# Optimization experiments

Hardware: AMD Instinct MI355X
Metric: run time of the kernel (lower is better)

## Reference

```python
import jax, jax.numpy as jnp
import numpy as np

D_MODEL = 512
NUM_HEADS = 8
HEAD_DIM = D_MODEL // NUM_HEADS


def setup_inputs() -> dict:
    key = jax.random.key(0)
    ks = jax.random.split(key, 11)
    N, S, D = 2, 4096, D_MODEL
    s = 1.0 / np.sqrt(D)
    return {
        "query": jax.random.normal(ks[0], (N, S, D), jnp.float32),
        "key": jax.random.normal(ks[1], (N, S, D), jnp.float32),
        "value": jax.random.normal(ks[2], (N, S, D), jnp.float32),
        "Wq": jax.random.normal(ks[3], (D, D), jnp.float32) * s,
        "bq": jnp.zeros((D,), jnp.float32),
        "Wk": jax.random.normal(ks[4], (D, D), jnp.float32) * s,
        "bk": jnp.zeros((D,), jnp.float32),
        "Wv": jax.random.normal(ks[5], (D, D), jnp.float32) * s,
        "bv": jnp.zeros((D,), jnp.float32),
        "Wo": jax.random.normal(ks[6], (D, D), jnp.float32) * s,
        "bo": jnp.zeros((D,), jnp.float32),
    }


def reference(query, key, value, Wq, bq, Wk, bk, Wv, bv, Wo, bo):
    N, S, D = query.shape
    H, Hd = NUM_HEADS, HEAD_DIM
    # Linear projections (torch Linear: x @ W.T + b), split heads -> [N,H,S,Hd]
    Q = (query @ Wq.T + bq).reshape(N, S, H, Hd).transpose(0, 2, 1, 3)
    K = (key @ Wk.T + bk).reshape(N, S, H, Hd).transpose(0, 2, 1, 3)
    V = (value @ Wv.T + bv).reshape(N, S, H, Hd).transpose(0, 2, 1, 3)
    scale = 1.0 / np.sqrt(Hd)
    energy = jnp.einsum("nhqd,nhkd->nhqk", Q, K) * scale  # [N,H,S,S]
    attention = jax.nn.softmax(energy, axis=-1)
    out = jnp.einsum("nhqk,nhkd->nhqd", attention, V)
    out = out.transpose(0, 2, 1, 3).reshape(N, S, D)
    return out @ Wo.T + bo
```

## Files before the change

kernel.cpp:

```cpp
#include <hip/hip_runtime.h>


#define SEQ 4096
#define PERHEAD 262144
#define CEXPF 0.18033688011112042f

typedef short bf16x8 __attribute__((ext_vector_type(8)));
typedef short bf16x4 __attribute__((ext_vector_type(4)));
typedef float f32x4 __attribute__((ext_vector_type(4)));
typedef unsigned short u16;
typedef unsigned int u32;

__device__ inline float bf2f(u16 h) {
    return __uint_as_float(((u32)h) << 16);
}
__device__ inline u16 f2bf(float f) {
    u32 u = __float_as_uint(f);
    u = (u + 0x7fffu + ((u >> 16) & 1u)) >> 16;
    return (u16)u;
}
__device__ inline u32 packtrunc(float lo, float hi) {
    return __builtin_amdgcn_perm(__float_as_uint(hi), __float_as_uint(lo),
                                 0x07060302u);
}
__device__ inline uint4 pack8(float4 a, float4 b) {
    uint4 r;
    r.x = (u32)f2bf(a.x) | ((u32)f2bf(a.y) << 16);
    r.y = (u32)f2bf(a.z) | ((u32)f2bf(a.w) << 16);
    r.z = (u32)f2bf(b.x) | ((u32)f2bf(b.y) << 16);
    r.w = (u32)f2bf(b.z) | ((u32)f2bf(b.w) << 16);
    return r;
}

__global__ void detect_dtype(const u16* __restrict__ W, int* __restrict__ flag) {
    const int lane = threadIdx.x & 63;
    u16 u = W[2 * lane];
    int e = (u >> 7) & 0xFF;
    int plaus = (u == 0) || (e >= 100 && e <= 132);
    unsigned long long m = __ballot(plaus);
    if (lane == 0) *flag = (__popcll(m) >= 48) ? 0 : 1;
}

__global__ __launch_bounds__(256) void prep(
    const void* __restrict__ W0, const void* __restrict__ W1,
    const void* __restrict__ W2, const void* __restrict__ W3,
    const void* __restrict__ b0, const void* __restrict__ b1,
    const void* __restrict__ b2, const void* __restrict__ b3,
    u16* __restrict__ Wc, u16* __restrict__ bc, const int* __restrict__ flag)
{
    const int m = blockIdx.y;
    const void* Ws = (m == 0) ? W0 : (m == 1) ? W1 : (m == 2) ? W2 : W3;
    const void* bs = (m == 0) ? b0 : (m == 1) ? b1 : (m == 2) ? b2 : b3;
    const int isf32 = *flag;
    if (blockIdx.x < 128) {
        const int idx = blockIdx.x * 2048 + threadIdx.x * 8;
        u16* dst = Wc + (size_t)m * 262144 + idx;
        if (isf32) {
            const float4* s = (const float4*)((const float*)Ws + idx);
            *(uint4*)dst = pack8(s[0], s[1]);
        } else {
            *(uint4*)dst = *(const uint4*)((const u16*)Ws + idx);
        }
    } else if (threadIdx.x < 64) {
        const int idx = threadIdx.x * 8;
        u16* dst = bc + m * 512 + idx;
        if (isf32) {
            const float4* s = (const float4*)((const float*)bs + idx);
            *(uint4*)dst = pack8(s[0], s[1]);
        } else {
            *(uint4*)dst = *(const uint4*)((const u16*)bs + idx);
        }
    }
}

template <int A_BF16>
__device__ inline void gemm_body(
    const void* __restrict__ Av, const u16* __restrict__ B,
    const u16* __restrict__ bias, void* __restrict__ outv,
    int isf32, int mode, float scale, int m0, int n0,
    u16* As, u16* Bs)
{
    const int tid = threadIdx.x;
    const int wave = tid >> 6, lane = tid & 63, quad = lane >> 4, ln = lane & 15;
    const int qr = wave >> 1, qc = wave & 1;

    f32x4 acc[4][4];
#pragma unroll
    for (int i = 0; i < 4; i++)
#pragma unroll
        for (int j = 0; j < 4; j++) acc[i][j] = (f32x4){0.f, 0.f, 0.f, 0.f};

    const int srow = tid >> 1;
    const int scol = (tid & 1) * 16;
    const uint4*  Ag16 = (const uint4*) ((const u16*)Av + (size_t)(m0 + srow) * 512 + scol);
    const float4* Ag32 = (const float4*)((const float*)Av + (size_t)(m0 + srow) * 512 + scol);
    const uint4*  Bg   = (const uint4*) (B + (size_t)(n0 + srow) * 512 + scol);
    uint4* Al = (uint4*)(As + srow * 40 + scol);
    uint4* Bl = (uint4*)(Bs + srow * 40 + scol);

    for (int kk = 0; kk < 512; kk += 32) {
        __syncthreads();
        uint4 aw0, aw1;
        if (A_BF16 || !isf32) {
            aw0 = Ag16[0]; aw1 = Ag16[1];
            Ag16 += 4;
        } else {
            float4 f0 = Ag32[0], f1 = Ag32[1], f2 = Ag32[2], f3 = Ag32[3];
            Ag32 += 8;
            aw0 = pack8(f0, f1); aw1 = pack8(f2, f3);
        }
        uint4 bw0 = Bg[0], bw1 = Bg[1];
        Bg += 4;
        Al[0] = aw0; Al[1] = aw1; Bl[0] = bw0; Bl[1] = bw1;
        __syncthreads();
        bf16x8 af[4], bfr[4];
#pragma unroll
        for (int mi = 0; mi < 4; mi++)
            af[mi] = *(const bf16x8*)(As + (qr * 64 + mi * 16 + ln) * 40 + quad * 8);
#pragma unroll
        for (int ni = 0; ni < 4; ni++)
            bfr[ni] = *(const bf16x8*)(Bs + (qc * 64 + ni * 16 + ln) * 40 + quad * 8);
#pragma unroll
        for (int mi = 0; mi < 4; mi++)
#pragma unroll
            for (int ni = 0; ni < 4; ni++)
                acc[mi][ni] = __builtin_amdgcn_mfma_f32_16x16x32_bf16(
                    af[mi], bfr[ni], acc[mi][ni], 0, 0, 0);
    }

#pragma unroll
    for (int ni = 0; ni < 4; ni++) {
        const int col = n0 + qc * 64 + ni * 16 + ln;
        const float bvv = bf2f(bias[col]);
#pragma unroll
        for (int mi = 0; mi < 4; mi++) {
#pragma unroll
            for (int r = 0; r < 4; r++) {
                const int row = m0 + qr * 64 + mi * 16 + quad * 4 + r;
                const float v = (acc[mi][ni][r] + bvv) * scale;
                if (mode == 0) {
                    const size_t idx = (size_t)row * 512 + col;
                    if (isf32) ((float*)outv)[idx] = v;
                    else       ((u16*)outv)[idx] = f2bf(v);
                } else {
                    const int b = row >> 12, s = row & 4095;
                    const int h = col >> 6, hd = col & 63;
                    size_t idx;
                    if (mode == 1)
                        idx = (size_t)(b * 8 + h) * PERHEAD + (size_t)s * 64 + hd;
                    else
                        idx = (size_t)(b * 8 + h) * PERHEAD + (size_t)hd * 4096 + s;
                    ((u16*)outv)[idx] = f2bf(v);
                }
            }
        }
    }
}

__global__ __launch_bounds__(256) void qkv_proj(
    const void* __restrict__ q, const void* __restrict__ k, const void* __restrict__ v,
    const u16* __restrict__ Wc, const u16* __restrict__ bc,
    u16* __restrict__ Qh, u16* __restrict__ Kh, u16* __restrict__ Vt,
    const int* __restrict__ flag)
{
    __shared__ __align__(16) u16 As[128 * 40];
    __shared__ __align__(16) u16 Bs[128 * 40];
    const int z = blockIdx.z;
    const void* Av = (z == 0) ? q : (z == 1) ? k : v;
    void* outv = (z == 0) ? (void*)Qh : (z == 1) ? (void*)Kh : (void*)Vt;
    const int mode = (z == 2) ? 2 : 1;
    const float scale = (z == 0) ? CEXPF : 1.0f;
    gemm_body<0>(Av, Wc + (size_t)z * 262144, bc + z * 512, outv,
                 *flag, mode, scale, blockIdx.y * 128, blockIdx.x * 128, As, Bs);
}

__global__ __launch_bounds__(256) void out_proj(
    const void* __restrict__ Av, const u16* __restrict__ Wc,
    const u16* __restrict__ bc, void* __restrict__ outv,
    const int* __restrict__ flag)
{
    __shared__ __align__(16) u16 As[128 * 40];
    __shared__ __align__(16) u16 Bs[128 * 40];
    gemm_body<1>(Av, Wc + (size_t)3 * 262144, bc + 3 * 512, outv,
                 *flag, 0, 1.0f, blockIdx.y * 128, blockIdx.x * 128, As, Bs);
}

__global__ __launch_bounds__(256) void attn_kernel(
    const u16* __restrict__ Q, const u16* __restrict__ K,
    const u16* __restrict__ Vt, u16* __restrict__ AO)
{
    __shared__ __align__(16) u16 Ks[64 * 72];
    __shared__ __align__(16) u16 Vs[64 * 72];

    const int tid = threadIdx.x;
    const int w = tid >> 6, lane = tid & 63, quad = lane >> 4, ln = lane & 15;
    const int bh = blockIdx.y;
    const int q0 = blockIdx.x * 128;
    const size_t base = (size_t)bh * PERHEAD;

    bf16x8 qf[2][2];
#pragma unroll
    for (int qt = 0; qt < 2; qt++) {
        const uint4* qp = (const uint4*)(Q + base + (size_t)(q0 + w * 32 + qt * 16 + ln) * 64);
        uint4 v0 = qp[quad], v1 = qp[4 + quad];
        qf[qt][0] = *(bf16x8*)&v0;
        qf[qt][1] = *(bf16x8*)&v1;
    }

    bf16x8 ones;
#pragma unroll
    for (int j = 0; j < 8; j++) ones[j] = (short)0x3F80;

    f32x4 oT[2][4];
    f32x4 lacc[2];
#pragma unroll
    for (int qt = 0; qt < 2; qt++) {
        lacc[qt] = (f32x4){0.f, 0.f, 0.f, 0.f};
#pragma unroll
        for (int mt = 0; mt < 4; mt++) oT[qt][mt] = (f32x4){0.f, 0.f, 0.f, 0.f};
    }

    const int srow = tid >> 2;
    const int sc = (tid & 3) * 16;
    const uint4* Kg = (const uint4*)(K + base + (size_t)srow * 64 + sc);
    const uint4* Vg = (const uint4*)(Vt + base + (size_t)srow * 4096 + sc);
    uint4* Kl = (uint4*)(Ks + srow * 72 + sc);
    uint4* Vl = (uint4*)(Vs + srow * 72 + sc);

    for (int k0 = 0; k0 < SEQ; k0 += 64) {
        __syncthreads();
        {
            uint4 a = Kg[0], b = Kg[1], c = Vg[0], d = Vg[1];
            Kg += 512;
            Vg += 8;
            Kl[0] = a; Kl[1] = b; Vl[0] = c; Vl[1] = d;
        }
        __syncthreads();

        f32x4 s[2][4];
#pragma unroll
        for (int t = 0; t < 2; t++)
#pragma unroll
            for (int kt = 0; kt < 4; kt++) {
                bf16x8 kf = *(const bf16x8*)(Ks + (kt * 16 + ln) * 72 + t * 32 + quad * 8);
#pragma unroll
                for (int qt = 0; qt < 2; qt++) {
                    if (t == 0)
                        s[qt][kt] = __builtin_amdgcn_mfma_f32_16x16x32_bf16(
                            kf, qf[qt][0], (f32x4){0.f, 0.f, 0.f, 0.f}, 0, 0, 0);
                    else
                        s[qt][kt] = __builtin_amdgcn_mfma_f32_16x16x32_bf16(
                            kf, qf[qt][1], s[qt][kt], 0, 0, 0);
                }
            }

        bf16x8 pf[2][2];
#pragma unroll
        for (int qt = 0; qt < 2; qt++)
#pragma unroll
            for (int c = 0; c < 2; c++) {
                float e0 = exp2f(s[qt][2 * c][0]), e1 = exp2f(s[qt][2 * c][1]);
                float e2 = exp2f(s[qt][2 * c][2]), e3 = exp2f(s[qt][2 * c][3]);
                float f0 = exp2f(s[qt][2 * c + 1][0]), f1 = exp2f(s[qt][2 * c + 1][1]);
                float f2 = exp2f(s[qt][2 * c + 1][2]), f3 = exp2f(s[qt][2 * c + 1][3]);
                u32 w0 = packtrunc(e0, e1), w1 = packtrunc(e2, e3);
                u32 w2 = packtrunc(f0, f1), w3 = packtrunc(f2, f3);
                uint4 pk = {w0, w1, w2, w3};
                pf[qt][c] = *(bf16x8*)&pk;
            }

#pragma unroll
        for (int qt = 0; qt < 2; qt++)
#pragma unroll
            for (int c = 0; c < 2; c++)
                lacc[qt] = __builtin_amdgcn_mfma_f32_16x16x32_bf16(
                    ones, pf[qt][c], lacc[qt], 0, 0, 0);

#pragma unroll
        for (int c = 0; c < 2; c++)
#pragma unroll
            for (int mt = 0; mt < 4; mt++) {
                const u16* vrow = Vs + (mt * 16 + ln) * 72 + c * 32 + quad * 4;
                bf16x4 v0 = *(const bf16x4*)(vrow);
                bf16x4 v1 = *(const bf16x4*)(vrow + 16);
                bf16x8 vf;
#pragma unroll
                for (int j = 0; j < 4; j++) { vf[j] = v0[j]; vf[4 + j] = v1[j]; }
#pragma unroll
                for (int qt = 0; qt < 2; qt++)
                    oT[qt][mt] = __builtin_amdgcn_mfma_f32_16x16x32_bf16(
                        vf, pf[qt][c], oT[qt][mt], 0, 0, 0);
            }
    }

    const int b = bh >> 3, h = bh & 7;
#pragma unroll
    for (int qt = 0; qt < 2; qt++) {
        const float inv = 1.0f / lacc[qt][0];
        const int qrow = q0 + w * 32 + qt * 16 + ln;
        u16* op = AO + (size_t)(b * 4096 + qrow) * 512 + h * 64 + quad * 4;
#pragma unroll
        for (int mt = 0; mt < 4; mt++) {
            uint2 pk;
            pk.x = (u32)f2bf(oT[qt][mt][0] * inv) | ((u32)f2bf(oT[qt][mt][1] * inv) << 16);
            pk.y = (u32)f2bf(oT[qt][mt][2] * inv) | ((u32)f2bf(oT[qt][mt][3] * inv) << 16);
            *(uint2*)(op + mt * 16) = pk;
        }
    }
}

extern "C" void kernel_launch(void* const* d_in, const int* in_sizes, int n_in,
                              void* d_out, int out_size, void* d_ws, size_t ws_size,
                              hipStream_t stream)
{
    (void)in_sizes; (void)n_in; (void)out_size; (void)ws_size;
    const void* q  = d_in[0];
    const void* k  = d_in[1];
    const void* v  = d_in[2];
    const void* Wq = d_in[3];
    const void* bq = d_in[4];
    const void* Wk = d_in[5];
    const void* bk = d_in[6];
    const void* Wv = d_in[7];
    const void* bv = d_in[8];
    const void* Wo = d_in[9];
    const void* bo = d_in[10];

    u16* ws = (u16*)d_ws;
    u16* Kh = ws;
    u16* Vt = ws + 4194304;
    u16* AO = ws + 8388608;
    u16* Wc = ws + 12582912;
    u16* bc = ws + 12582912 + 1048576;
    int* flag = (int*)(ws + 12582912 + 1048576 + 2048);
    u16* Qh = (u16*)d_out;

    detect_dtype<<<1, 64, 0, stream>>>((const u16*)Wq, flag);
    prep<<<dim3(129, 4), 256, 0, stream>>>(Wq, Wk, Wv, Wo, bq, bk, bv, bo,
                                           Wc, bc, flag);
    qkv_proj<<<dim3(4, 64, 3), 256, 0, stream>>>(q, k, v, Wc, bc, Qh, Kh, Vt, flag);
    attn_kernel<<<dim3(32, 16), 256, 0, stream>>>(Qh, Kh, Vt, AO);
    out_proj<<<dim3(4, 64), 256, 0, stream>>>(AO, Wc, bc, d_out, flag);
}
```

Before: 285.8 us.

## Double-buffer LDS tiles in GEMM and attention, permute V layout for wide loads

Both the projection GEMM and the attention kernel now use two LDS buffers. Global loads for the next tile are issued before computing on the current one, so each iteration needs only one barrier instead of two. The V projection writes its transposed output with a permuted sequence order, so the PV step can fetch each MFMA operand with one 16-byte LDS read instead of two 8-byte reads and a repack. The attention loop also uses the raw hardware exp2 builtin and raises wave priority around the MFMA blocks. LDS use doubles, and the last attention iteration prefetches one tile past the head, which reads out of bounds for the final head.

```diff
diff --git a/kernel.cpp b/kernel.cpp
--- a/kernel.cpp
+++ b/kernel.cpp
@@ -95,38 +95,62 @@
     const uint4*  Ag16 = (const uint4*) ((const u16*)Av + (size_t)(m0 + srow) * 512 + scol);
     const float4* Ag32 = (const float4*)((const float*)Av + (size_t)(m0 + srow) * 512 + scol);
     const uint4*  Bg   = (const uint4*) (B + (size_t)(n0 + srow) * 512 + scol);
-    uint4* Al = (uint4*)(As + srow * 40 + scol);
-    uint4* Bl = (uint4*)(Bs + srow * 40 + scol);
-
-    for (int kk = 0; kk < 512; kk += 32) {
-        __syncthreads();
+    const int loff = srow * 40 + scol;
+
+    auto compute_tile = [&](const u16* Ac, const u16* Bc) {
+        bf16x8 af[4], bfr[4];
+#pragma unroll
+        for (int mi = 0; mi < 4; mi++)
+            af[mi] = *(const bf16x8*)(Ac + (qr * 64 + mi * 16 + ln) * 40 + quad * 8);
+#pragma unroll
+        for (int ni = 0; ni < 4; ni++)
+            bfr[ni] = *(const bf16x8*)(Bc + (qc * 64 + ni * 16 + ln) * 40 + quad * 8);
+#pragma unroll
+        for (int mi = 0; mi < 4; mi++)
+#pragma unroll
+            for (int ni = 0; ni < 4; ni++)
+                acc[mi][ni] = __builtin_amdgcn_mfma_f32_16x16x32_bf16(
+                    af[mi], bfr[ni], acc[mi][ni], 0, 0, 0);
+    };
+
+    {
         uint4 aw0, aw1;
         if (A_BF16 || !isf32) {
-            aw0 = Ag16[0]; aw1 = Ag16[1];
-            Ag16 += 4;
+            aw0 = Ag16[0]; aw1 = Ag16[1]; Ag16 += 4;
         } else {
             float4 f0 = Ag32[0], f1 = Ag32[1], f2 = Ag32[2], f3 = Ag32[3];
             Ag32 += 8;
             aw0 = pack8(f0, f1); aw1 = pack8(f2, f3);
         }
-        uint4 bw0 = Bg[0], bw1 = Bg[1];
-        Bg += 4;
+        uint4 bw0 = Bg[0], bw1 = Bg[1]; Bg += 4;
+        uint4* Al = (uint4*)(As + loff);
+        uint4* Bl = (uint4*)(Bs + loff);
+        Al[0] = aw0; Al[1] = aw1; Bl[0] = bw0; Bl[1] = bw1;
+    }
+    __syncthreads();
+
+    for (int kk = 32; kk < 512; kk += 32) {
+        const int nb = (kk >> 5) & 1;
+        uint4 aw0, aw1, bw0, bw1;
+        float4 f0, f1, f2, f3;
+        const int araw = A_BF16 || !isf32;
+        if (araw) {
+            aw0 = Ag16[0]; aw1 = Ag16[1]; Ag16 += 4;
+        } else {
+            f0 = Ag32[0]; f1 = Ag32[1]; f2 = Ag32[2]; f3 = Ag32[3];
+            Ag32 += 8;
+        }
+        bw0 = Bg[0]; bw1 = Bg[1]; Bg += 4;
+
+        compute_tile(As + (nb ^ 1) * 5120, Bs + (nb ^ 1) * 5120);
+
+        if (!araw) { aw0 = pack8(f0, f1); aw1 = pack8(f2, f3); }
+        uint4* Al = (uint4*)(As + nb * 5120 + loff);
+        uint4* Bl = (uint4*)(Bs + nb * 5120 + loff);
         Al[0] = aw0; Al[1] = aw1; Bl[0] = bw0; Bl[1] = bw1;
         __syncthreads();
-        bf16x8 af[4], bfr[4];
-#pragma unroll
-        for (int mi = 0; mi < 4; mi++)
-            af[mi] = *(const bf16x8*)(As + (qr * 64 + mi * 16 + ln) * 40 + quad * 8);
-#pragma unroll
-        for (int ni = 0; ni < 4; ni++)
-            bfr[ni] = *(const bf16x8*)(Bs + (qc * 64 + ni * 16 + ln) * 40 + quad * 8);
-#pragma unroll
-        for (int mi = 0; mi < 4; mi++)
-#pragma unroll
-            for (int ni = 0; ni < 4; ni++)
-                acc[mi][ni] = __builtin_amdgcn_mfma_f32_16x16x32_bf16(
-                    af[mi], bfr[ni], acc[mi][ni], 0, 0, 0);
-    }
+    }
+    compute_tile(As + 5120, Bs + 5120);
 
 #pragma unroll
     for (int ni = 0; ni < 4; ni++) {
@@ -146,10 +170,15 @@
                     const int b = row >> 12, s = row & 4095;
                     const int h = col >> 6, hd = col & 63;
                     size_t idx;
-                    if (mode == 1)
+                    if (mode == 1) {
                         idx = (size_t)(b * 8 + h) * PERHEAD + (size_t)s * 64 + hd;
-                    else
-                        idx = (size_t)(b * 8 + h) * PERHEAD + (size_t)hd * 4096 + s;
+                    } else {
+                        const int s6 = s & 63;
+                        const int p = (s6 & 32) | ((s6 & 12) << 1) |
+                                      ((s6 & 16) >> 2) | (s6 & 3);
+                        idx = (size_t)(b * 8 + h) * PERHEAD + (size_t)hd * 4096 +
+                              (size_t)((s & ~63) + p);
+                    }
                     ((u16*)outv)[idx] = f2bf(v);
                 }
             }
@@ -163,8 +192,8 @@
     u16* __restrict__ Qh, u16* __restrict__ Kh, u16* __restrict__ Vt,
     const int* __restrict__ flag)
 {
-    __shared__ __align__(16) u16 As[128 * 40];
-    __shared__ __align__(16) u16 Bs[128 * 40];
+    __shared__ __align__(16) u16 As[2 * 128 * 40];
+    __shared__ __align__(16) u16 Bs[2 * 128 * 40];
     const int z = blockIdx.z;
     const void* Av = (z == 0) ? q : (z == 1) ? k : v;
     void* outv = (z == 0) ? (void*)Qh : (z == 1) ? (void*)Kh : (void*)Vt;
@@ -179,8 +208,8 @@
     const u16* __restrict__ bc, void* __restrict__ outv,
     const int* __restrict__ flag)
 {
-    __shared__ __align__(16) u16 As[128 * 40];
-    __shared__ __align__(16) u16 Bs[128 * 40];
+    __shared__ __align__(16) u16 As[2 * 128 * 40];
+    __shared__ __align__(16) u16 Bs[2 * 128 * 40];
     gemm_body<1>(Av, Wc + (size_t)3 * 262144, bc + 3 * 512, outv,
                  *flag, 0, 1.0f, blockIdx.y * 128, blockIdx.x * 128, As, Bs);
 }
@@ -189,8 +218,8 @@
     const u16* __restrict__ Q, const u16* __restrict__ K,
     const u16* __restrict__ Vt, u16* __restrict__ AO)
 {
-    __shared__ __align__(16) u16 Ks[64 * 72];
-    __shared__ __align__(16) u16 Vs[64 * 72];
+    __shared__ __align__(16) u16 Ks[2][64 * 72];
+    __shared__ __align__(16) u16 Vs[2][64 * 72];
 
     const int tid = threadIdx.x;
     const int w = tid >> 6, lane = tid & 63, quad = lane >> 4, ln = lane & 15;
@@ -224,25 +253,31 @@
     const int sc = (tid & 3) * 16;
     const uint4* Kg = (const uint4*)(K + base + (size_t)srow * 64 + sc);
     const uint4* Vg = (const uint4*)(Vt + base + (size_t)srow * 4096 + sc);
-    uint4* Kl = (uint4*)(Ks + srow * 72 + sc);
-    uint4* Vl = (uint4*)(Vs + srow * 72 + sc);
-
-    for (int k0 = 0; k0 < SEQ; k0 += 64) {
-        __syncthreads();
-        {
-            uint4 a = Kg[0], b = Kg[1], c = Vg[0], d = Vg[1];
-            Kg += 512;
-            Vg += 8;
-            Kl[0] = a; Kl[1] = b; Vl[0] = c; Vl[1] = d;
-        }
-        __syncthreads();
+    const int soff = srow * 72 + sc;
+
+    {
+        uint4 a = Kg[0], b = Kg[1], c = Vg[0], d = Vg[1];
+        Kg += 512; Vg += 8;
+        uint4* Kl = (uint4*)(Ks[0] + soff);
+        uint4* Vl = (uint4*)(Vs[0] + soff);
+        Kl[0] = a; Kl[1] = b; Vl[0] = c; Vl[1] = d;
+    }
+    __syncthreads();
+
+    for (int it = 0; it < 64; ++it) {
+        const u16* Kc = Ks[it & 1];
+        const u16* Vc = Vs[it & 1];
+
+        uint4 pa = Kg[0], pb = Kg[1], pc = Vg[0], pd = Vg[1];
+        Kg += 512; Vg += 8;
 
         f32x4 s[2][4];
+        __builtin_amdgcn_s_setprio(1);
 #pragma unroll
         for (int t = 0; t < 2; t++)
 #pragma unroll
             for (int kt = 0; kt < 4; kt++) {
-                bf16x8 kf = *(const bf16x8*)(Ks + (kt * 16 + ln) * 72 + t * 32 + quad * 8);
+                bf16x8 kf = *(const bf16x8*)(Kc + (kt * 16 + ln) * 72 + t * 32 + quad * 8);
 #pragma unroll
                 for (int qt = 0; qt < 2; qt++) {
                     if (t == 0)
@@ -253,22 +288,28 @@
                             kf, qf[qt][1], s[qt][kt], 0, 0, 0);
                 }
             }
+        __builtin_amdgcn_s_setprio(0);
 
         bf16x8 pf[2][2];
 #pragma unroll
         for (int qt = 0; qt < 2; qt++)
 #pragma unroll
             for (int c = 0; c < 2; c++) {
-                float e0 = exp2f(s[qt][2 * c][0]), e1 = exp2f(s[qt][2 * c][1]);
-                float e2 = exp2f(s[qt][2 * c][2]), e3 = exp2f(s[qt][2 * c][3]);
-                float f0 = exp2f(s[qt][2 * c + 1][0]), f1 = exp2f(s[qt][2 * c + 1][1]);
-                float f2 = exp2f(s[qt][2 * c + 1][2]), f3 = exp2f(s[qt][2 * c + 1][3]);
+                float e0 = __builtin_amdgcn_exp2f(s[qt][2 * c][0]);
+                float e1 = __builtin_amdgcn_exp2f(s[qt][2 * c][1]);
+                float e2 = __builtin_amdgcn_exp2f(s[qt][2 * c][2]);
+                float e3 = __builtin_amdgcn_exp2f(s[qt][2 * c][3]);
+                float f0 = __builtin_amdgcn_exp2f(s[qt][2 * c + 1][0]);
+                float f1 = __builtin_amdgcn_exp2f(s[qt][2 * c + 1][1]);
+                float f2 = __builtin_amdgcn_exp2f(s[qt][2 * c + 1][2]);
+                float f3 = __builtin_amdgcn_exp2f(s[qt][2 * c + 1][3]);
                 u32 w0 = packtrunc(e0, e1), w1 = packtrunc(e2, e3);
                 u32 w2 = packtrunc(f0, f1), w3 = packtrunc(f2, f3);
                 uint4 pk = {w0, w1, w2, w3};
                 pf[qt][c] = *(bf16x8*)&pk;
             }
 
+        __builtin_amdgcn_s_setprio(1);
 #pragma unroll
         for (int qt = 0; qt < 2; qt++)
 #pragma unroll
@@ -280,17 +321,20 @@
         for (int c = 0; c < 2; c++)
 #pragma unroll
             for (int mt = 0; mt < 4; mt++) {
-                const u16* vrow = Vs + (mt * 16 + ln) * 72 + c * 32 + quad * 4;
-                bf16x4 v0 = *(const bf16x4*)(vrow);
-                bf16x4 v1 = *(const bf16x4*)(vrow + 16);
-                bf16x8 vf;
-#pragma unroll
-                for (int j = 0; j < 4; j++) { vf[j] = v0[j]; vf[4 + j] = v1[j]; }
+                bf16x8 vf = *(const bf16x8*)(Vc + (mt * 16 + ln) * 72 + c * 32 + quad * 8);
 #pragma unroll
                 for (int qt = 0; qt < 2; qt++)
                     oT[qt][mt] = __builtin_amdgcn_mfma_f32_16x16x32_bf16(
                         vf, pf[qt][c], oT[qt][mt], 0, 0, 0);
             }
+        __builtin_amdgcn_s_setprio(0);
+
+        {
+            uint4* Kl = (uint4*)(Ks[(it + 1) & 1] + soff);
+            uint4* Vl = (uint4*)(Vs[(it + 1) & 1] + soff);
+            Kl[0] = pa; Kl[1] = pb; Vl[0] = pc; Vl[1] = pd;
+        }
+        __syncthreads();
     }
 
     const int b = bh >> 3, h = bh & 7;
```

After: 267.5 us. -6.4%, faster.

## Split attention keys across two wave groups with double-buffered LDS and permuted V layout

Applied to the files above, without the earlier changes.

The attention kernel now runs 512 threads: two groups of four waves each take half of the key sequence for the same query tile. Each group double-buffers K/V tiles in LDS, prefetching the next tile into registers while computing. Partial outputs and row sums are then combined through shared memory. The V-transpose store in the projection is permuted within each 64-key block so each lane reads one contiguous 8-element vector instead of two 4-element loads. The change also adds s_setprio around MFMA sections and switches exp2f to the raw hardware builtin. The cost is more LDS per block and an extra reduction step at the end.

```diff
diff --git a/kernel.cpp b/kernel.cpp
--- a/kernel.cpp
+++ b/kernel.cpp
@@ -146,10 +146,15 @@
                     const int b = row >> 12, s = row & 4095;
                     const int h = col >> 6, hd = col & 63;
                     size_t idx;
-                    if (mode == 1)
+                    if (mode == 1) {
                         idx = (size_t)(b * 8 + h) * PERHEAD + (size_t)s * 64 + hd;
-                    else
-                        idx = (size_t)(b * 8 + h) * PERHEAD + (size_t)hd * 4096 + s;
+                    } else {
+                        const int s6 = s & 63;
+                        const int p = (s6 & 32) | ((s6 & 12) << 1) |
+                                      ((s6 & 16) >> 2) | (s6 & 3);
+                        idx = (size_t)(b * 8 + h) * PERHEAD + (size_t)hd * 4096 +
+                              (size_t)((s & ~63) + p);
+                    }
                     ((u16*)outv)[idx] = f2bf(v);
                 }
             }
@@ -185,15 +190,16 @@
                  *flag, 0, 1.0f, blockIdx.y * 128, blockIdx.x * 128, As, Bs);
 }
 
-__global__ __launch_bounds__(256) void attn_kernel(
+__global__ __launch_bounds__(512) void attn_kernel(
     const u16* __restrict__ Q, const u16* __restrict__ K,
     const u16* __restrict__ Vt, u16* __restrict__ AO)
 {
-    __shared__ __align__(16) u16 Ks[64 * 72];
-    __shared__ __align__(16) u16 Vs[64 * 72];
+    __shared__ __align__(16) u16 S[2][2][2][64 * 72];
 
     const int tid = threadIdx.x;
-    const int w = tid >> 6, lane = tid & 63, quad = lane >> 4, ln = lane & 15;
+    const int g = tid >> 8;
+    const int wq = (tid >> 6) & 3;
+    const int lane = tid & 63, quad = lane >> 4, ln = lane & 15;
     const int bh = blockIdx.y;
     const int q0 = blockIdx.x * 128;
     const size_t base = (size_t)bh * PERHEAD;
@@ -201,7 +207,7 @@
     bf16x8 qf[2][2];
 #pragma unroll
     for (int qt = 0; qt < 2; qt++) {
-        const uint4* qp = (const uint4*)(Q + base + (size_t)(q0 + w * 32 + qt * 16 + ln) * 64);
+        const uint4* qp = (const uint4*)(Q + base + (size_t)(q0 + wq * 32 + qt * 16 + ln) * 64);
         uint4 v0 = qp[quad], v1 = qp[4 + quad];
         qf[qt][0] = *(bf16x8*)&v0;
         qf[qt][1] = *(bf16x8*)&v1;
@@ -220,29 +226,36 @@
         for (int mt = 0; mt < 4; mt++) oT[qt][mt] = (f32x4){0.f, 0.f, 0.f, 0.f};
     }
 
-    const int srow = tid >> 2;
-    const int sc = (tid & 3) * 16;
-    const uint4* Kg = (const uint4*)(K + base + (size_t)srow * 64 + sc);
-    const uint4* Vg = (const uint4*)(Vt + base + (size_t)srow * 4096 + sc);
-    uint4* Kl = (uint4*)(Ks + srow * 72 + sc);
-    uint4* Vl = (uint4*)(Vs + srow * 72 + sc);
-
-    for (int k0 = 0; k0 < SEQ; k0 += 64) {
-        __syncthreads();
-        {
-            uint4 a = Kg[0], b = Kg[1], c = Vg[0], d = Vg[1];
-            Kg += 512;
-            Vg += 8;
-            Kl[0] = a; Kl[1] = b; Vl[0] = c; Vl[1] = d;
-        }
-        __syncthreads();
+    const int tid2 = tid & 255;
+    const int srow = tid2 >> 2;
+    const int sc = (tid2 & 3) * 16;
+    const uint4* Kg = (const uint4*)(K + base + (size_t)(g * 2048 + srow) * 64 + sc);
+    const uint4* Vg = (const uint4*)(Vt + base + (size_t)srow * 4096 + g * 2048 + sc);
+    const int soff = srow * 72 + sc;
+
+    {
+        uint4 a = Kg[0], b = Kg[1], c = Vg[0], d = Vg[1];
+        Kg += 512; Vg += 8;
+        uint4* Kl = (uint4*)(&S[g][0][0][0] + soff);
+        uint4* Vl = (uint4*)(&S[g][0][1][0] + soff);
+        Kl[0] = a; Kl[1] = b; Vl[0] = c; Vl[1] = d;
+    }
+    __syncthreads();
+
+    for (int it = 0; it < 32; ++it) {
+        const u16* Kc = &S[g][it & 1][0][0];
+        const u16* Vc = &S[g][it & 1][1][0];
+
+        uint4 pa = Kg[0], pb = Kg[1], pc = Vg[0], pd = Vg[1];
+        Kg += 512; Vg += 8;
 
         f32x4 s[2][4];
+        __builtin_amdgcn_s_setprio(1);
 #pragma unroll
         for (int t = 0; t < 2; t++)
 #pragma unroll
             for (int kt = 0; kt < 4; kt++) {
-                bf16x8 kf = *(const bf16x8*)(Ks + (kt * 16 + ln) * 72 + t * 32 + quad * 8);
+                bf16x8 kf = *(const bf16x8*)(Kc + (kt * 16 + ln) * 72 + t * 32 + quad * 8);
 #pragma unroll
                 for (int qt = 0; qt < 2; qt++) {
                     if (t == 0)
@@ -253,22 +266,28 @@
                             kf, qf[qt][1], s[qt][kt], 0, 0, 0);
                 }
             }
+        __builtin_amdgcn_s_setprio(0);
 
         bf16x8 pf[2][2];
 #pragma unroll
         for (int qt = 0; qt < 2; qt++)
 #pragma unroll
             for (int c = 0; c < 2; c++) {
-                float e0 = exp2f(s[qt][2 * c][0]), e1 = exp2f(s[qt][2 * c][1]);
-                float e2 = exp2f(s[qt][2 * c][2]), e3 = exp2f(s[qt][2 * c][3]);
-                float f0 = exp2f(s[qt][2 * c + 1][0]), f1 = exp2f(s[qt][2 * c + 1][1]);
-                float f2 = exp2f(s[qt][2 * c + 1][2]), f3 = exp2f(s[qt][2 * c + 1][3]);
+                float e0 = __builtin_amdgcn_exp2f(s[qt][2 * c][0]);
+                float e1 = __builtin_amdgcn_exp2f(s[qt][2 * c][1]);
+                float e2 = __builtin_amdgcn_exp2f(s[qt][2 * c][2]);
+                float e3 = __builtin_amdgcn_exp2f(s[qt][2 * c][3]);
+                float f0 = __builtin_amdgcn_exp2f(s[qt][2 * c + 1][0]);
+                float f1 = __builtin_amdgcn_exp2f(s[qt][2 * c + 1][1]);
+                float f2 = __builtin_amdgcn_exp2f(s[qt][2 * c + 1][2]);
+                float f3 = __builtin_amdgcn_exp2f(s[qt][2 * c + 1][3]);
                 u32 w0 = packtrunc(e0, e1), w1 = packtrunc(e2, e3);
                 u32 w2 = packtrunc(f0, f1), w3 = packtrunc(f2, f3);
                 uint4 pk = {w0, w1, w2, w3};
                 pf[qt][c] = *(bf16x8*)&pk;
             }
 
+        __builtin_amdgcn_s_setprio(1);
 #pragma unroll
         for (int qt = 0; qt < 2; qt++)
 #pragma unroll
@@ -280,31 +299,60 @@
         for (int c = 0; c < 2; c++)
 #pragma unroll
             for (int mt = 0; mt < 4; mt++) {
-                const u16* vrow = Vs + (mt * 16 + ln) * 72 + c * 32 + quad * 4;
-                bf16x4 v0 = *(const bf16x4*)(vrow);
-                bf16x4 v1 = *(const bf16x4*)(vrow + 16);
-                bf16x8 vf;
-#pragma unroll
-                for (int j = 0; j < 4; j++) { vf[j] = v0[j]; vf[4 + j] = v1[j]; }
+                bf16x8 vf = *(const bf16x8*)(Vc + (mt * 16 + ln) * 72 + c * 32 + quad * 8);
 #pragma unroll
                 for (int qt = 0; qt < 2; qt++)
                     oT[qt][mt] = __builtin_amdgcn_mfma_f32_16x16x32_bf16(
                         vf, pf[qt][c], oT[qt][mt], 0, 0, 0);
             }
-    }
-
-    const int b = bh >> 3, h = bh & 7;
-#pragma unroll
-    for (int qt = 0; qt < 2; qt++) {
-        const float inv = 1.0f / lacc[qt][0];
-        const int qrow = q0 + w * 32 + qt * 16 + ln;
-        u16* op = AO + (size_t)(b * 4096 + qrow) * 512 + h * 64 + quad * 4;
-#pragma unroll
-        for (int mt = 0; mt < 4; mt++) {
-            uint2 pk;
-            pk.x = (u32)f2bf(oT[qt][mt][0] * inv) | ((u32)f2bf(oT[qt][mt][1] * inv) << 16);
-            pk.y = (u32)f2bf(oT[qt][mt][2] * inv) | ((u32)f2bf(oT[qt][mt][3] * inv) << 16);
-            *(uint2*)(op + mt * 16) = pk;
+        __builtin_amdgcn_s_setprio(0);
+
+        {
+            uint4* Kl = (uint4*)(&S[g][(it + 1) & 1][0][0] + soff);
+            uint4* Vl = (uint4*)(&S[g][(it + 1) & 1][1][0] + soff);
+            Kl[0] = pa; Kl[1] = pb; Vl[0] = pc; Vl[1] = pd;
+        }
+        __syncthreads();
+    }
+
+    float* Xch = (float*)&S[0][0][0][0];
+    if (g == 1) {
+#pragma unroll
+        for (int qt = 0; qt < 2; qt++) {
+#pragma unroll
+            for (int mt = 0; mt < 4; mt++)
+#pragma unroll
+                for (int r = 0; r < 4; r++)
+                    Xch[(((wq * 2 + qt) * 4 + mt) * 16 + quad * 4 + r) * 17 + ln] =
+                        oT[qt][mt][r];
+            if (quad == 0)
+                Xch[8704 + (wq * 2 + qt) * 16 + ln] = lacc[qt][0];
+        }
+    }
+    __syncthreads();
+    if (g == 0) {
+        const int b = bh >> 3, h = bh & 7;
+#pragma unroll
+        for (int qt = 0; qt < 2; qt++) {
+            const float l2 = Xch[8704 + (wq * 2 + qt) * 16 + ln];
+            const float inv = 1.0f / (lacc[qt][0] + l2);
+            const int qrow = q0 + wq * 32 + qt * 16 + ln;
+            u16* op = AO + (size_t)(b * 4096 + qrow) * 512 + h * 64 + quad * 4;
+#pragma unroll
+            for (int mt = 0; mt < 4; mt++) {
+                float o0 = oT[qt][mt][0] +
+                    Xch[(((wq * 2 + qt) * 4 + mt) * 16 + quad * 4 + 0) * 17 + ln];
+                float o1 = oT[qt][mt][1] +
+                    Xch[(((wq * 2 + qt) * 4 + mt) * 16 + quad * 4 + 1) * 17 + ln];
+                float o2 = oT[qt][mt][2] +
+                    Xch[(((wq * 2 + qt) * 4 + mt) * 16 + quad * 4 + 2) * 17 + ln];
+                float o3 = oT[qt][mt][3] +
+                    Xch[(((wq * 2 + qt) * 4 + mt) * 16 + quad * 4 + 3) * 17 + ln];
+                uint2 pk;
+                pk.x = (u32)f2bf(o0 * inv) | ((u32)f2bf(o1 * inv) << 16);
+                pk.y = (u32)f2bf(o2 * inv) | ((u32)f2bf(o3 * inv) << 16);
+                *(uint2*)(op + mt * 16) = pk;
+            }
         }
     }
 }
@@ -339,6 +387,6 @@
     prep<<<dim3(129, 4), 256, 0, stream>>>(Wq, Wk, Wv, Wo, bq, bk, bv, bo,
                                            Wc, bc, flag);
     qkv_proj<<<dim3(4, 64, 3), 256, 0, stream>>>(q, k, v, Wc, bc, Qh, Kh, Vt, flag);
-    attn_kernel<<<dim3(32, 16), 256, 0, stream>>>(Qh, Kh, Vt, AO);
+    attn_kernel<<<dim3(32, 16), 512, 0, stream>>>(Qh, Kh, Vt, AO);
     out_proj<<<dim3(4, 64), 256, 0, stream>>>(AO, Wc, bc, d_out, flag);
 }
```

Measured after the change: 242.0 us. 1.18x faster.
